# Kernel tuning notes

Measured on AMD Instinct MI355X. Metric: run time of the kernel, lower is better.

## Reference

```python
import jax, jax.numpy as jnp
import numpy as np

B, S, D, H, DFF = 4, 2048, 1024, 16, 4096
DK = D // H
EPS = 1e-5


def setup_inputs() -> dict:
    key = jax.random.key(0)
    ks = jax.random.split(key, 10)
    s = 0.02
    return {
        "x": jax.random.normal(ks[0], (B, S, D), jnp.float32),
        "wq": jax.random.normal(ks[1], (D, D), jnp.float32) * s,
        "wk": jax.random.normal(ks[2], (D, D), jnp.float32) * s,
        "wv": jax.random.normal(ks[3], (D, D), jnp.float32) * s,
        "wo": jax.random.normal(ks[4], (D, D), jnp.float32) * s,
        "w1": jax.random.normal(ks[5], (D, DFF), jnp.float32) * s,
        "b1": jnp.zeros((DFF,), jnp.float32),
        "w2": jax.random.normal(ks[6], (DFF, D), jnp.float32) * s,
        "b2": jnp.zeros((D,), jnp.float32),
        "g1": jnp.ones((D,), jnp.float32),
        "be1": jnp.zeros((D,), jnp.float32),
        "g2": jnp.ones((D,), jnp.float32),
        "be2": jnp.zeros((D,), jnp.float32),
    }


def _layernorm(x, g, b):
    mu = jnp.mean(x, axis=-1, keepdims=True)
    var = jnp.mean(jnp.square(x - mu), axis=-1, keepdims=True)
    return (x - mu) * jax.lax.rsqrt(var + EPS) * g + b


def reference(x, wq, wk, wv, wo, w1, b1, w2, b2, g1, be1, g2, be2):
    # --- self-attention block (pre-LN) ---
    residual = x
    h = _layernorm(x, g1, be1)
    q = (h @ wq).reshape(B, S, H, DK).transpose(0, 2, 1, 3)  # [B,H,S,DK]
    k = (h @ wk).reshape(B, S, H, DK).transpose(0, 2, 1, 3)
    v = (h @ wv).reshape(B, S, H, DK).transpose(0, 2, 1, 3)
    scores = jnp.einsum("bhqd,bhkd->bhqk", q, k) / jnp.sqrt(jnp.float32(DK))
    weights = jax.nn.softmax(scores, axis=-1)
    weights = jnp.nan_to_num(weights, nan=0.0)
    attn = jnp.einsum("bhqk,bhkd->bhqd", weights, v)
    attn = attn.transpose(0, 2, 1, 3).reshape(B, S, D)
    x = residual + attn @ wo
    # --- FFN block (pre-LN) ---
    residual = x
    h = _layernorm(x, g2, be2)
    h = jax.nn.relu(h @ w1 + b1) @ w2 + b2
    return residual + h
```

## Files before the change

kernel.cpp:

```cpp
#include <hip/hip_runtime.h>
#include <stdint.h>

#define B_ 4
#define S_ 2048
#define D_ 1024
#define H_ 16
#define DFF_ 4096
#define QSTR 3072

typedef __attribute__((ext_vector_type(8))) short short8;
typedef __attribute__((ext_vector_type(4))) short short4v;
typedef __attribute__((ext_vector_type(4))) float floatx4;

typedef const __attribute__((address_space(1))) void* gas_ptr;
typedef __attribute__((address_space(3))) void* las_ptr;

__device__ __forceinline__ short f2bf(float f) {
  union { float f; uint32_t u; } v; v.f = f;
  uint32_t r = v.u + 0x7fffu + ((v.u >> 16) & 1u);
  return (short)(r >> 16);
}

__global__ __launch_bounds__(256) void ln_kernel(
    const float* __restrict__ x, const float* __restrict__ g,
    const float* __restrict__ be, short* __restrict__ out)
{
  const int row = blockIdx.x;
  const int tid = threadIdx.x;
  const float4 v = ((const float4*)(x + (size_t)row * D_))[tid];
  float s1 = v.x + v.y + v.z + v.w;
  float s2 = v.x*v.x + v.y*v.y + v.z*v.z + v.w*v.w;
#pragma unroll
  for (int off = 1; off < 64; off <<= 1) {
    s1 += __shfl_xor(s1, off);
    s2 += __shfl_xor(s2, off);
  }
  __shared__ float r1[4], r2[4];
  if ((tid & 63) == 0) { r1[tid >> 6] = s1; r2[tid >> 6] = s2; }
  __syncthreads();
  s1 = r1[0] + r1[1] + r1[2] + r1[3];
  s2 = r2[0] + r2[1] + r2[2] + r2[3];
  const float mu = s1 * (1.0f / D_);
  const float var = s2 * (1.0f / D_) - mu * mu;
  const float rs = rsqrtf(var + 1e-5f);
  const float4 gv = ((const float4*)g)[tid];
  const float4 bv = ((const float4*)be)[tid];
  short4v o;
  o.x = f2bf((v.x - mu) * rs * gv.x + bv.x);
  o.y = f2bf((v.y - mu) * rs * gv.y + bv.y);
  o.z = f2bf((v.z - mu) * rs * gv.z + bv.z);
  o.w = f2bf((v.w - mu) * rs * gv.w + bv.w);
  *(short4v*)&out[(size_t)row * D_ + tid * 4] = o;
}

__global__ __launch_bounds__(256) void transpose_cast(
    const float* __restrict__ in, short* __restrict__ out, int R, int C)
{
  __shared__ float tile[32][33];
  const int tx = threadIdx.x & 31, ty = threadIdx.x >> 5;
  const int r0 = blockIdx.y * 32, c0 = blockIdx.x * 32;
#pragma unroll
  for (int i = 0; i < 4; i++)
    tile[ty + i * 8][tx] = in[(size_t)(r0 + ty + i * 8) * C + c0 + tx];
  __syncthreads();
#pragma unroll
  for (int i = 0; i < 4; i++)
    out[(size_t)(c0 + ty + i * 8) * R + r0 + tx] = f2bf(tile[tx][ty + i * 8]);
}

__global__ __launch_bounds__(256) void transpose_v(
    const short* __restrict__ in, short* __restrict__ out)
{
  __shared__ short t[64 * 66];
  const int b = blockIdx.z;
  const int s0 = blockIdx.x * 64, c0 = blockIdx.y * 64;
  const int tid = threadIdx.x;
  const int lrow = tid >> 5, lp = tid & 31;
#pragma unroll
  for (int i = 0; i < 8; i++) {
    const int s = lrow + i * 8;
    *(uint32_t*)&t[s * 66 + lp * 2] =
        *(const uint32_t*)&in[((size_t)b * S_ + s0 + s) * D_ + c0 + lp * 2];
  }
  __syncthreads();
#pragma unroll
  for (int i = 0; i < 8; i++) {
    const int cc = lrow + i * 8;
    const uint32_t lo = (uint16_t)t[(lp * 2) * 66 + cc];
    const uint32_t hi = (uint16_t)t[(lp * 2 + 1) * 66 + cc];
    *(uint32_t*)&out[((size_t)b * D_ + c0 + cc) * S_ + s0 + lp * 2] = lo | (hi << 16);
  }
}

__global__ __launch_bounds__(256, 4) void gemm_bt(
    const short* __restrict__ A, const short* __restrict__ Bt,
    float* __restrict__ outf, short* __restrict__ outb,
    short* __restrict__ outbK, short* __restrict__ outbV,
    const float* __restrict__ bias, const float* __restrict__ resid,
    int M, int N, int K, int do_relu, int split, int group)
{
  __shared__ short As[2 * 128 * 32];
  __shared__ short Bs[2 * 128 * 32];
  const int tid = threadIdx.x;
  const int wave = tid >> 6;
  const int lane = tid & 63;
  const int quad = lane >> 4;
  const int l16 = lane & 15;

  const uint32_t nblk = gridDim.x;
  const uint32_t pid = blockIdx.y * nblk + blockIdx.x;
  const uint32_t nig = (uint32_t)group * nblk;
  const uint32_t gid = pid / nig;
  const uint32_t within = pid - gid * nig;
  const uint32_t bm = gid * group + within % group;
  const uint32_t bn = within / group;
  const int tm = bm * 128;
  const int tn = bn * 128;

  const int wm = (wave & 1) * 64;
  const int wn = (wave >> 1) * 64;
  const int srow = lane >> 2;
  const int scol = (lane & 3) * 8;

  floatx4 acc[4][4];
#pragma unroll
  for (int i = 0; i < 4; i++)
#pragma unroll
    for (int j = 0; j < 4; j++) acc[i][j] = floatx4{0.f, 0.f, 0.f, 0.f};

  const short* gA0 = A + (size_t)(tm + wave * 32 + srow) * K + scol;
  const short* gB0 = Bt + (size_t)(tn + wave * 32 + srow) * K + scol;

  for (int kt = 0; kt < K; kt += 64) {
    __syncthreads();
    __builtin_amdgcn_global_load_lds((gas_ptr)(gA0 + kt),                      (las_ptr)(&As[wave * 1024]),        16, 0, 0);
    __builtin_amdgcn_global_load_lds((gas_ptr)(gA0 + kt + (size_t)16 * K),     (las_ptr)(&As[wave * 1024 + 512]),  16, 0, 0);
    __builtin_amdgcn_global_load_lds((gas_ptr)(gB0 + kt),                      (las_ptr)(&Bs[wave * 1024]),        16, 0, 0);
    __builtin_amdgcn_global_load_lds((gas_ptr)(gB0 + kt + (size_t)16 * K),     (las_ptr)(&Bs[wave * 1024 + 512]),  16, 0, 0);
    __builtin_amdgcn_global_load_lds((gas_ptr)(gA0 + kt + 32),                 (las_ptr)(&As[4096 + wave * 1024]),       16, 0, 0);
    __builtin_amdgcn_global_load_lds((gas_ptr)(gA0 + kt + 32 + (size_t)16 * K),(las_ptr)(&As[4096 + wave * 1024 + 512]), 16, 0, 0);
    __builtin_amdgcn_global_load_lds((gas_ptr)(gB0 + kt + 32),                 (las_ptr)(&Bs[4096 + wave * 1024]),       16, 0, 0);
    __builtin_amdgcn_global_load_lds((gas_ptr)(gB0 + kt + 32 + (size_t)16 * K),(las_ptr)(&Bs[4096 + wave * 1024 + 512]), 16, 0, 0);
    __syncthreads();

#pragma unroll
    for (int ksub = 0; ksub < 2; ksub++) {
      const int hb = ksub * 4096;
      short8 af[4], bfv[4];
#pragma unroll
      for (int mi = 0; mi < 4; mi++)
        af[mi] = *(const short8*)&As[hb + (wm + mi * 16 + l16) * 32 + quad * 8];
#pragma unroll
      for (int ni = 0; ni < 4; ni++)
        bfv[ni] = *(const short8*)&Bs[hb + (wn + ni * 16 + l16) * 32 + quad * 8];
#pragma unroll
      for (int mi = 0; mi < 4; mi++)
#pragma unroll
        for (int ni = 0; ni < 4; ni++)
          acc[mi][ni] = __builtin_amdgcn_mfma_f32_16x16x32_bf16(af[mi], bfv[ni], acc[mi][ni], 0, 0, 0);
    }
  }

  short* ob = outb;
  int Nst = N;
  int cbase = tn;
  if (split) {
    const int part = tn >> 10;
    ob = (part == 0) ? outb : (part == 1) ? outbK : outbV;
    Nst = D_;
    cbase = tn & (D_ - 1);
  }

#pragma unroll
  for (int mi = 0; mi < 4; mi++) {
    const int row0 = tm + wm + mi * 16 + quad * 4;
#pragma unroll
    for (int ni = 0; ni < 4; ni++) {
      const int col = tn + wn + ni * 16 + l16;
      const int cst = cbase + wn + ni * 16 + l16;
      const float bv = bias ? bias[col] : 0.0f;
#pragma unroll
      for (int r = 0; r < 4; r++) {
        const size_t idx = (size_t)(row0 + r) * Nst + cst;
        float v = acc[mi][ni][r] + bv;
        if (do_relu) v = fmaxf(v, 0.0f);
        if (resid) v += resid[idx];
        if (outf) outf[idx] = v;
        if (ob) ob[idx] = f2bf(v);
      }
    }
  }
}

__global__ __launch_bounds__(256, 4) void gemm_bt_n64(
    const short* __restrict__ A, const short* __restrict__ Bt,
    float* __restrict__ outf,
    const float* __restrict__ bias, const float* __restrict__ resid,
    int M, int N, int K, int group)
{
  __shared__ short As[2 * 128 * 32];
  __shared__ short Bs[2 * 64 * 32];
  const int tid = threadIdx.x;
  const int wave = tid >> 6;
  const int lane = tid & 63;
  const int quad = lane >> 4;
  const int l16 = lane & 15;

  const uint32_t nblk = gridDim.x;
  const uint32_t pid = blockIdx.y * nblk + blockIdx.x;
  const uint32_t nig = (uint32_t)group * nblk;
  const uint32_t gid = pid / nig;
  const uint32_t within = pid - gid * nig;
  const uint32_t bm = gid * group + within % group;
  const uint32_t bn = within / group;
  const int tm = bm * 128;
  const int tn = bn * 64;

  const int wm = (wave & 1) * 64;
  const int wn = (wave >> 1) * 32;
  const int srow = lane >> 2;
  const int scol = (lane & 3) * 8;

  floatx4 acc[4][2];
#pragma unroll
  for (int i = 0; i < 4; i++)
#pragma unroll
    for (int j = 0; j < 2; j++) acc[i][j] = floatx4{0.f, 0.f, 0.f, 0.f};

  const short* gA0 = A + (size_t)(tm + wave * 32 + srow) * K + scol;
  const short* gB0 = Bt + (size_t)(tn + wave * 16 + srow) * K + scol;

  for (int kt = 0; kt < K; kt += 64) {
    __syncthreads();
    __builtin_amdgcn_global_load_lds((gas_ptr)(gA0 + kt),                      (las_ptr)(&As[wave * 1024]),        16, 0, 0);
    __builtin_amdgcn_global_load_lds((gas_ptr)(gA0 + kt + (size_t)16 * K),     (las_ptr)(&As[wave * 1024 + 512]),  16, 0, 0);
    __builtin_amdgcn_global_load_lds((gas_ptr)(gA0 + kt + 32),                 (las_ptr)(&As[4096 + wave * 1024]),       16, 0, 0);
    __builtin_amdgcn_global_load_lds((gas_ptr)(gA0 + kt + 32 + (size_t)16 * K),(las_ptr)(&As[4096 + wave * 1024 + 512]), 16, 0, 0);
    __builtin_amdgcn_global_load_lds((gas_ptr)(gB0 + kt),      (las_ptr)(&Bs[wave * 512]),        16, 0, 0);
    __builtin_amdgcn_global_load_lds((gas_ptr)(gB0 + kt + 32), (las_ptr)(&Bs[2048 + wave * 512]), 16, 0, 0);
    __syncthreads();

#pragma unroll
    for (int ksub = 0; ksub < 2; ksub++) {
      const int ha = ksub * 4096;
      const int hbv = ksub * 2048;
      short8 af[4], bfv[2];
#pragma unroll
      for (int mi = 0; mi < 4; mi++)
        af[mi] = *(const short8*)&As[ha + (wm + mi * 16 + l16) * 32 + quad * 8];
#pragma unroll
      for (int ni = 0; ni < 2; ni++)
        bfv[ni] = *(const short8*)&Bs[hbv + (wn + ni * 16 + l16) * 32 + quad * 8];
#pragma unroll
      for (int mi = 0; mi < 4; mi++)
#pragma unroll
        for (int ni = 0; ni < 2; ni++)
          acc[mi][ni] = __builtin_amdgcn_mfma_f32_16x16x32_bf16(af[mi], bfv[ni], acc[mi][ni], 0, 0, 0);
    }
  }

#pragma unroll
  for (int mi = 0; mi < 4; mi++) {
    const int row0 = tm + wm + mi * 16 + quad * 4;
#pragma unroll
    for (int ni = 0; ni < 2; ni++) {
      const int col = tn + wn + ni * 16 + l16;
      const float bv = bias ? bias[col] : 0.0f;
#pragma unroll
      for (int r = 0; r < 4; r++) {
        const size_t idx = (size_t)(row0 + r) * N + col;
        float v = acc[mi][ni][r] + bv;
        if (resid) v += resid[idx];
        outf[idx] = v;
      }
    }
  }
}

#define LSTR 68
__global__ __launch_bounds__(256) void attn_kernel(
    const short* __restrict__ qb, const short* __restrict__ kb,
    const short* __restrict__ vtb, short* __restrict__ attb)
{
  __shared__ short Ks[64 * LSTR];
  __shared__ short Vts[64 * LSTR];
  __shared__ short Ps[128 * LSTR];

  const int tid = threadIdx.x;
  const int wave = tid >> 6, lane = tid & 63, quad = lane >> 4, l16 = lane & 15;
  const int qt = blockIdx.x, bh = blockIdx.y;
  const int b = bh >> 4, h = bh & 15;
  const size_t rowbase = (size_t)b * S_;
  const int hcol = h * 64;
  const int r = tid >> 2, c = (tid & 3) * 16;

  short8 qa[2][2];
#pragma unroll
  for (int qs = 0; qs < 2; qs++) {
    const short* gq = qb + (rowbase + qt * 128 + qs * 64 + wave * 16 + l16) * D_ + hcol + quad * 8;
    short8 t0 = *(const short8*)gq;
    short8 t1 = *(const short8*)(gq + 32);
#pragma unroll
    for (int i = 0; i < 8; i++) {
      const float f0 = __uint_as_float(((uint32_t)(uint16_t)t0[i]) << 16) * 0.18033688f;
      const float f1 = __uint_as_float(((uint32_t)(uint16_t)t1[i]) << 16) * 0.18033688f;
      t0[i] = (short)((__float_as_uint(f0) + 0x8000u) >> 16);
      t1[i] = (short)((__float_as_uint(f1) + 0x8000u) >> 16);
    }
    qa[qs][0] = t0;
    qa[qs][1] = t1;
  }

  float l_run[2][4];
  floatx4 Of[2][4];
#pragma unroll
  for (int qs = 0; qs < 2; qs++)
#pragma unroll
    for (int rr = 0; rr < 4; rr++) { l_run[qs][rr] = 0.f; }
#pragma unroll
  for (int qs = 0; qs < 2; qs++)
#pragma unroll
    for (int nd = 0; nd < 4; nd++) Of[qs][nd] = floatx4{0.f, 0.f, 0.f, 0.f};

  const short* gk0 = kb + (rowbase + r) * D_ + hcol + c;
  const short* gv0 = vtb + ((size_t)bh * 64 + r) * S_ + c;

  short8 kr0 = *(const short8*)gk0, kr1 = *(const short8*)(gk0 + 8);
  short8 vr0 = *(const short8*)gv0, vr1 = *(const short8*)(gv0 + 8);

  for (int kt = 0; kt < S_; kt += 64) {
    __syncthreads();
    *(short8*)&Ks[r * LSTR + c]      = kr0;
    *(short8*)&Ks[r * LSTR + c + 8]  = kr1;
    *(short8*)&Vts[r * LSTR + c]     = vr0;
    *(short8*)&Vts[r * LSTR + c + 8] = vr1;
    __syncthreads();

    {
      const int ktn = (kt + 64 < S_) ? kt + 64 : 0;
      const short* gk = gk0 + (size_t)ktn * D_;
      const short* gv = gv0 + ktn;
      kr0 = *(const short8*)gk; kr1 = *(const short8*)(gk + 8);
      vr0 = *(const short8*)gv; vr1 = *(const short8*)(gv + 8);
    }

#pragma unroll
    for (int nk = 0; nk < 4; nk++) {
      const short8 kf0 = *(const short8*)&Ks[(nk * 16 + l16) * LSTR + quad * 8];
      const short8 kf1 = *(const short8*)&Ks[(nk * 16 + l16) * LSTR + 32 + quad * 8];
#pragma unroll
      for (int qs = 0; qs < 2; qs++) {
        floatx4 s = floatx4{0.f, 0.f, 0.f, 0.f};
        s = __builtin_amdgcn_mfma_f32_16x16x32_bf16(qa[qs][0], kf0, s, 0, 0, 0);
        s = __builtin_amdgcn_mfma_f32_16x16x32_bf16(qa[qs][1], kf1, s, 0, 0, 0);
#pragma unroll
        for (int rr = 0; rr < 4; rr++) {
          const float p = __builtin_amdgcn_exp2f(s[rr]);
          l_run[qs][rr] += p;
          Ps[(qs * 64 + wave * 16 + quad * 4 + rr) * LSTR + nk * 16 + l16] =
              (short)((__float_as_uint(p) + 0x8000u) >> 16);
        }
      }
    }

    asm volatile("" ::: "memory");
    short8 pa[2][2];
#pragma unroll
    for (int qs = 0; qs < 2; qs++) {
      pa[qs][0] = *(const short8*)&Ps[(qs * 64 + wave * 16 + l16) * LSTR + quad * 8];
      pa[qs][1] = *(const short8*)&Ps[(qs * 64 + wave * 16 + l16) * LSTR + 32 + quad * 8];
    }
#pragma unroll
    for (int nd = 0; nd < 4; nd++) {
      const short8 vf0 = *(const short8*)&Vts[(nd * 16 + l16) * LSTR + quad * 8];
      const short8 vf1 = *(const short8*)&Vts[(nd * 16 + l16) * LSTR + 32 + quad * 8];
#pragma unroll
      for (int qs = 0; qs < 2; qs++) {
        Of[qs][nd] = __builtin_amdgcn_mfma_f32_16x16x32_bf16(pa[qs][0], vf0, Of[qs][nd], 0, 0, 0);
        Of[qs][nd] = __builtin_amdgcn_mfma_f32_16x16x32_bf16(pa[qs][1], vf1, Of[qs][nd], 0, 0, 0);
      }
    }
  }

#pragma unroll
  for (int off = 1; off < 16; off <<= 1)
#pragma unroll
    for (int qs = 0; qs < 2; qs++)
#pragma unroll
      for (int rr = 0; rr < 4; rr++) l_run[qs][rr] += __shfl_xor(l_run[qs][rr], off);
#pragma unroll
  for (int qs = 0; qs < 2; qs++) {
    float inv[4];
#pragma unroll
    for (int rr = 0; rr < 4; rr++) inv[rr] = 1.0f / l_run[qs][rr];
#pragma unroll
    for (int nd = 0; nd < 4; nd++)
#pragma unroll
      for (int rr = 0; rr < 4; rr++) {
        const int qrow = qt * 128 + qs * 64 + wave * 16 + quad * 4 + rr;
        const int col = hcol + nd * 16 + l16;
        attb[(rowbase + qrow) * D_ + col] = f2bf(Of[qs][nd][rr] * inv[rr]);
      }
  }
}

extern "C" void kernel_launch(void* const* d_in, const int* in_sizes, int n_in,
                              void* d_out, int out_size, void* d_ws, size_t ws_size,
                              hipStream_t stream) {
  const float* x   = (const float*)d_in[0];
  const float* wq  = (const float*)d_in[1];
  const float* wk  = (const float*)d_in[2];
  const float* wv  = (const float*)d_in[3];
  const float* wo  = (const float*)d_in[4];
  const float* w1  = (const float*)d_in[5];
  const float* b1  = (const float*)d_in[6];
  const float* w2  = (const float*)d_in[7];
  const float* b2  = (const float*)d_in[8];
  const float* g1  = (const float*)d_in[9];
  const float* be1 = (const float*)d_in[10];
  const float* g2  = (const float*)d_in[11];
  const float* be2 = (const float*)d_in[12];
  float* out = (float*)d_out;

  const size_t MROWS = (size_t)B_ * S_;
  char* p = (char*)d_ws;
  auto take = [&](size_t bytes) { char* r = p; p += (bytes + 255) & ~(size_t)255; return r; };
  short* hb    = (short*)take(MROWS * D_ * 2);
  short* h2b   = (short*)take(MROWS * D_ * 2);
  short* qbuf  = (short*)take(MROWS * D_ * 2);
  short* kbuf  = (short*)take(MROWS * D_ * 2);
  short* vbuf  = (short*)take(MROWS * D_ * 2);
  short* attb  = (short*)take(MROWS * D_ * 2);
  short* ffb   = (short*)take(MROWS * DFF_ * 2);
  short* wqkvT = (short*)take((size_t)3 * D_ * D_ * 2);
  short* woT   = (short*)take((size_t)D_ * D_ * 2);
  short* w1T   = (short*)take((size_t)D_ * DFF_ * 2);
  short* w2T   = (short*)take((size_t)DFF_ * D_ * 2);
  float* x1    = (float*)take(MROWS * D_ * 4);
  short* vtb   = hb;

  transpose_cast<<<dim3(D_ / 32, D_ / 32), 256, 0, stream>>>(wq, wqkvT, D_, D_);
  transpose_cast<<<dim3(D_ / 32, D_ / 32), 256, 0, stream>>>(wk, wqkvT + (size_t)D_ * D_, D_, D_);
  transpose_cast<<<dim3(D_ / 32, D_ / 32), 256, 0, stream>>>(wv, wqkvT + (size_t)2 * D_ * D_, D_, D_);
  transpose_cast<<<dim3(D_ / 32, D_ / 32), 256, 0, stream>>>(wo, woT, D_, D_);
  transpose_cast<<<dim3(DFF_ / 32, D_ / 32), 256, 0, stream>>>(w1, w1T, D_, DFF_);
  transpose_cast<<<dim3(D_ / 32, DFF_ / 32), 256, 0, stream>>>(w2, w2T, DFF_, D_);

  ln_kernel<<<MROWS, 256, 0, stream>>>(x, g1, be1, hb);

  gemm_bt<<<dim3(QSTR / 128, MROWS / 128), 256, 0, stream>>>(
      hb, wqkvT, nullptr, qbuf, kbuf, vbuf, nullptr, nullptr, MROWS, QSTR, D_, 0, 1, 8);

  transpose_v<<<dim3(S_ / 64, D_ / 64, B_), 256, 0, stream>>>(vbuf, vtb);

  attn_kernel<<<dim3(S_ / 128, B_ * H_), 256, 0, stream>>>(qbuf, kbuf, vtb, attb);

  gemm_bt_n64<<<dim3(D_ / 64, MROWS / 128), 256, 0, stream>>>(
      attb, woT, x1, nullptr, x, MROWS, D_, D_, 8);

  ln_kernel<<<MROWS, 256, 0, stream>>>(x1, g2, be2, h2b);

  gemm_bt<<<dim3(DFF_ / 128, MROWS / 128), 256, 0, stream>>>(
      h2b, w1T, nullptr, ffb, nullptr, nullptr, b1, nullptr, MROWS, DFF_, D_, 1, 0, 8);

  gemm_bt_n64<<<dim3(D_ / 64, MROWS / 128), 256, 0, stream>>>(
      ffb, w2T, out, b2, x1, MROWS, D_, DFF_, 4);

  (void)in_sizes; (void)n_in; (void)out_size; (void)ws_size;
}
```

Before: 563.5 us.

## Fuse weight transposes into one launch and write V transposed from QKV GEMM

Six separate weight transpose-cast launches become a single kernel that picks its source matrix from the block index. The QKV GEMM epilogue now writes V directly in transposed [B, D, S] layout, so the standalone transpose_v kernel and its round trip through memory go away. The transposed V stores are 8-byte writes strided by S per column, which are less coalesced than the row-major stores they replace.

```diff
diff --git a/kernel.cpp b/kernel.cpp
--- a/kernel.cpp
+++ b/kernel.cpp
@@ -53,49 +53,44 @@
   *(short4v*)&out[(size_t)row * D_ + tid * 4] = o;
 }
 
-__global__ __launch_bounds__(256) void transpose_cast(
-    const float* __restrict__ in, short* __restrict__ out, int R, int C)
+__global__ __launch_bounds__(256) void transpose_all(
+    const float* __restrict__ wq, const float* __restrict__ wk,
+    const float* __restrict__ wv, const float* __restrict__ wo,
+    const float* __restrict__ w1, const float* __restrict__ w2,
+    short* __restrict__ wqkvT, short* __restrict__ woT,
+    short* __restrict__ w1T, short* __restrict__ w2T)
 {
-  __shared__ float tile[32][33];
+  const uint32_t pid = blockIdx.x;
+  const float* in; short* out;
+  int R, C, tile, xsh;
+  if (pid < 4096) {
+    const int which = pid >> 10; tile = pid & 1023;
+    R = 1024; C = 1024; xsh = 5;
+    in  = (which == 0) ? wq : (which == 1) ? wk : (which == 2) ? wv : wo;
+    out = (which == 3) ? woT : wqkvT + (size_t)which * 1024 * 1024;
+  } else if (pid < 8192) {
+    tile = pid - 4096; R = 1024; C = 4096; xsh = 7; in = w1; out = w1T;
+  } else {
+    tile = pid - 8192; R = 4096; C = 1024; xsh = 5; in = w2; out = w2T;
+  }
+  const int c0 = (tile & ((1 << xsh) - 1)) * 32;
+  const int r0 = (tile >> xsh) * 32;
+
+  __shared__ float t[32][33];
   const int tx = threadIdx.x & 31, ty = threadIdx.x >> 5;
-  const int r0 = blockIdx.y * 32, c0 = blockIdx.x * 32;
 #pragma unroll
   for (int i = 0; i < 4; i++)
-    tile[ty + i * 8][tx] = in[(size_t)(r0 + ty + i * 8) * C + c0 + tx];
+    t[ty + i * 8][tx] = in[(size_t)(r0 + ty + i * 8) * C + c0 + tx];
   __syncthreads();
 #pragma unroll
   for (int i = 0; i < 4; i++)
-    out[(size_t)(c0 + ty + i * 8) * R + r0 + tx] = f2bf(tile[tx][ty + i * 8]);
-}
-
-__global__ __launch_bounds__(256) void transpose_v(
-    const short* __restrict__ in, short* __restrict__ out)
-{
-  __shared__ short t[64 * 66];
-  const int b = blockIdx.z;
-  const int s0 = blockIdx.x * 64, c0 = blockIdx.y * 64;
-  const int tid = threadIdx.x;
-  const int lrow = tid >> 5, lp = tid & 31;
-#pragma unroll
-  for (int i = 0; i < 8; i++) {
-    const int s = lrow + i * 8;
-    *(uint32_t*)&t[s * 66 + lp * 2] =
-        *(const uint32_t*)&in[((size_t)b * S_ + s0 + s) * D_ + c0 + lp * 2];
-  }
-  __syncthreads();
-#pragma unroll
-  for (int i = 0; i < 8; i++) {
-    const int cc = lrow + i * 8;
-    const uint32_t lo = (uint16_t)t[(lp * 2) * 66 + cc];
-    const uint32_t hi = (uint16_t)t[(lp * 2 + 1) * 66 + cc];
-    *(uint32_t*)&out[((size_t)b * D_ + c0 + cc) * S_ + s0 + lp * 2] = lo | (hi << 16);
-  }
+    out[(size_t)(c0 + ty + i * 8) * R + r0 + tx] = f2bf(t[tx][ty + i * 8]);
 }
 
 __global__ __launch_bounds__(256, 4) void gemm_bt(
     const short* __restrict__ A, const short* __restrict__ Bt,
     float* __restrict__ outf, short* __restrict__ outb,
-    short* __restrict__ outbK, short* __restrict__ outbV,
+    short* __restrict__ outbK, short* __restrict__ vtT,
     const float* __restrict__ bias, const float* __restrict__ resid,
     int M, int N, int K, int do_relu, int split, int group)
 {
@@ -164,11 +159,30 @@
   short* ob = outb;
   int Nst = N;
   int cbase = tn;
+  int vpart = 0;
   if (split) {
     const int part = tn >> 10;
-    ob = (part == 0) ? outb : (part == 1) ? outbK : outbV;
+    if (part == 2) vpart = 1;
+    else ob = (part == 0) ? outb : outbK;
     Nst = D_;
     cbase = tn & (D_ - 1);
+  }
+
+  if (vpart) {
+#pragma unroll
+    for (int mi = 0; mi < 4; mi++) {
+      const int row0 = tm + wm + mi * 16 + quad * 4;
+      const int bb = row0 >> 11, s0r = row0 & 2047;
+#pragma unroll
+      for (int ni = 0; ni < 4; ni++) {
+        const int cst = cbase + wn + ni * 16 + l16;
+        short4v o;
+#pragma unroll
+        for (int r = 0; r < 4; r++) o[r] = f2bf(acc[mi][ni][r]);
+        *(short4v*)&vtT[((size_t)(bb << 10) + cst) * (size_t)S_ + s0r] = o;
+      }
+    }
+    return;
   }
 
 #pragma unroll
@@ -429,7 +443,7 @@
   short* h2b   = (short*)take(MROWS * D_ * 2);
   short* qbuf  = (short*)take(MROWS * D_ * 2);
   short* kbuf  = (short*)take(MROWS * D_ * 2);
-  short* vbuf  = (short*)take(MROWS * D_ * 2);
+  short* vtb   = (short*)take(MROWS * D_ * 2);
   short* attb  = (short*)take(MROWS * D_ * 2);
   short* ffb   = (short*)take(MROWS * DFF_ * 2);
   short* wqkvT = (short*)take((size_t)3 * D_ * D_ * 2);
@@ -437,21 +451,14 @@
   short* w1T   = (short*)take((size_t)D_ * DFF_ * 2);
   short* w2T   = (short*)take((size_t)DFF_ * D_ * 2);
   float* x1    = (float*)take(MROWS * D_ * 4);
-  short* vtb   = hb;
-
-  transpose_cast<<<dim3(D_ / 32, D_ / 32), 256, 0, stream>>>(wq, wqkvT, D_, D_);
-  transpose_cast<<<dim3(D_ / 32, D_ / 32), 256, 0, stream>>>(wk, wqkvT + (size_t)D_ * D_, D_, D_);
-  transpose_cast<<<dim3(D_ / 32, D_ / 32), 256, 0, stream>>>(wv, wqkvT + (size_t)2 * D_ * D_, D_, D_);
-  transpose_cast<<<dim3(D_ / 32, D_ / 32), 256, 0, stream>>>(wo, woT, D_, D_);
-  transpose_cast<<<dim3(DFF_ / 32, D_ / 32), 256, 0, stream>>>(w1, w1T, D_, DFF_);
-  transpose_cast<<<dim3(D_ / 32, DFF_ / 32), 256, 0, stream>>>(w2, w2T, DFF_, D_);
+
+  transpose_all<<<12288, 256, 0, stream>>>(wq, wk, wv, wo, w1, w2,
+                                           wqkvT, woT, w1T, w2T);
 
   ln_kernel<<<MROWS, 256, 0, stream>>>(x, g1, be1, hb);
 
   gemm_bt<<<dim3(QSTR / 128, MROWS / 128), 256, 0, stream>>>(
-      hb, wqkvT, nullptr, qbuf, kbuf, vbuf, nullptr, nullptr, MROWS, QSTR, D_, 0, 1, 8);
-
-  transpose_v<<<dim3(S_ / 64, D_ / 64, B_), 256, 0, stream>>>(vbuf, vtb);
+      hb, wqkvT, nullptr, qbuf, kbuf, vtb, nullptr, nullptr, MROWS, QSTR, D_, 0, 1, 8);
 
   attn_kernel<<<dim3(S_ / 128, B_ * H_), 256, 0, stream>>>(qbuf, kbuf, vtb, attb);
 
```

New measurement: 560.4 us. About the same (-0.6%).
